# Performance work log

Measured on AMD Instinct MI355X. Metric: run time of the kernel, lower is better.

Reference implementation:

```python
import jax, jax.numpy as jnp
import numpy as np

T = 512           # num_timestamps
D = 512           # video_embed_dim
V = 2048          # fmri_dim (voxels)
H = 128           # hidden_dim


def setup_inputs() -> dict:
    key = jax.random.key(0)
    k = jax.random.split(key, 8)
    s1 = 1.0 / np.sqrt(D)
    s2 = 1.0 / np.sqrt(H)
    return {
        "video_embeddings": jax.random.normal(k[0], (T, D), dtype=jnp.float32),
        # stacked per-voxel weights (torch Linear: y = x @ W.T + b; we store W already transposed as [in, out])
        "W1": jax.random.uniform(k[1], (V, D, H), jnp.float32, -s1, s1),
        "b1": jax.random.uniform(k[2], (V, H), jnp.float32, -s1, s1),
        "W2": jax.random.uniform(k[3], (V, H, H), jnp.float32, -s2, s2),
        "b2": jax.random.uniform(k[4], (V, H), jnp.float32, -s2, s2),
        "W3": jax.random.uniform(k[5], (V, H), jnp.float32, -s2, s2),
        "b3": jax.random.uniform(k[6], (V,), jnp.float32, -s2, s2),
    }


def reference(video_embeddings, W1, b1, W2, b2, W3, b3):
    # Per-voxel MLP expressed as batched GEMMs over the voxel axis.
    # Dropout is identity in eval mode.
    h = jax.nn.relu(jnp.einsum("td,vdh->tvh", video_embeddings, W1) + b1)  # [T,V,H]
    h = jax.nn.relu(jnp.einsum("tvh,vhg->tvg", h, W2) + b2)                 # [T,V,H]
    out = jnp.einsum("tvh,vh->tv", h, W3) + b3                               # [T,V]
    return out
```

## Files before the change

kernel.cpp:

```cpp
#include <hip/hip_runtime.h>
#include <hip/hip_bf16.h>

#define TT 512
#define DD 512
#define VV 2048
#define HH 128

typedef __attribute__((ext_vector_type(8))) short bf16x8;
typedef __attribute__((ext_vector_type(8))) unsigned short ushort8;
typedef __attribute__((ext_vector_type(4))) unsigned short ushort4v;
typedef __attribute__((ext_vector_type(4))) float f32x4;

__device__ __forceinline__ unsigned short f2bf(float f) {
  union { __hip_bfloat16 b; unsigned short u; } cv;
  cv.b = __float2bfloat16(f);
  return cv.u;
}

__device__ __forceinline__ void lds_barrier() {
  asm volatile("s_waitcnt lgkmcnt(0)\n\ts_barrier" ::: "memory");
}

__global__ void cvt_x_kernel(const float* __restrict__ x, unsigned short* __restrict__ xb) {
  const int i = blockIdx.x * blockDim.x + threadIdx.x;
  const float4 f = ((const float4*)x)[i];
  ushort4v u;
  u[0] = f2bf(f.x); u[1] = f2bf(f.y); u[2] = f2bf(f.z); u[3] = f2bf(f.w);
  ((ushort4v*)xb)[i] = u;
}

__global__ __launch_bounds__(512, 2)
void voxel_mlp_kernel(const unsigned short* __restrict__ Xb,
                      const float* __restrict__ W1,
                      const float* __restrict__ b1,
                      const float* __restrict__ W2,
                      const float* __restrict__ b2,
                      const float* __restrict__ W3,
                      const float* __restrict__ b3,
                      float* __restrict__ out) {
  __shared__ __align__(16) char LDS[65536];
  constexpr unsigned W2BASE = 0;
  constexpr unsigned R1     = 32768;
  constexpr unsigned H1BASE = 32768;

  const int v   = blockIdx.x;
  const int tid = threadIdx.x;
  const int w   = tid >> 6;
  const int l   = tid & 63;
  const int lg  = l >> 4;
  const int ll  = l & 15;

  const float* W1v = W1 + (size_t)v * DD * HH;
  const float* W2v = W2 + (size_t)v * HH * HH;

  const int stago = (lg * 8) * HH + w * 16 + ll;
  const unsigned short* Xrow[4];
#pragma unroll
  for (int mi = 0; mi < 4; ++mi)
    Xrow[mi] = Xb + (size_t)(w * 64 + mi * 16 + ll) * DD + lg * 8;

  float w1s[4][8];
  float w2s[2][8];
  bf16x8 aS[2][4];

#define ISSUE_W1(t, slot)                                         \
  { const float* gp = W1v + stago + (t) * 32 * HH;                \
    _Pragma("unroll") for (int j = 0; j < 8; ++j)                 \
      w1s[slot][j] = gp[j * HH]; }

#define ISSUE_W2(t, slot)                                         \
  { const float* gp = W2v + stago + (t) * 32 * HH;                \
    _Pragma("unroll") for (int j = 0; j < 8; ++j)                 \
      w2s[slot][j] = gp[j * HH]; }

#define ISSUE_A(st, slot)                                         \
  { _Pragma("unroll") for (int mi = 0; mi < 4; ++mi)              \
      aS[slot][mi] = *(const bf16x8*)(Xrow[mi] + (st) * 32); }

#define CVT_W1(slot, dstByte)                                     \
  { ushort8 u;                                                    \
    _Pragma("unroll") for (int j = 0; j < 8; ++j)                 \
      u[j] = f2bf(w1s[slot][j]);                                  \
    *(ushort8*)(&LDS[(dstByte) + (unsigned)w * 1024u + (unsigned)l * 16u]) = u; }

#define CVT_W2(slot, dstByte)                                     \
  { ushort8 u;                                                    \
    _Pragma("unroll") for (int j = 0; j < 8; ++j)                 \
      u[j] = f2bf(w2s[slot][j]);                                  \
    *(ushort8*)(&LDS[(dstByte) + (unsigned)w * 1024u + (unsigned)l * 16u]) = u; }

  ISSUE_A(0, 0);
  ISSUE_W1(0, 0);
  ISSUE_W1(1, 1);
  ISSUE_W1(2, 2);
  CVT_W1(0, R1 + 0u * 8192u);
  lds_barrier();

  f32x4 acc1[4][8];
#pragma unroll
  for (int mi = 0; mi < 4; ++mi)
#pragma unroll
    for (int n = 0; n < 8; ++n) acc1[mi][n] = f32x4{0.f, 0.f, 0.f, 0.f};

#pragma unroll
  for (int s = 0; s < 16; ++s) {
    if (s + 1 < 16) ISSUE_A(s + 1, (s + 1) & 1);
    if (s + 3 < 16) ISSUE_W1(s + 3, (s + 3) & 3);

#pragma unroll
    for (int n = 0; n < 8; ++n) {
      const bf16x8 b = *(const bf16x8*)(&LDS[R1 + (unsigned)(s & 3) * 8192u + (unsigned)n * 1024u + (unsigned)l * 16u]);
#pragma unroll
      for (int mi = 0; mi < 4; ++mi)
        acc1[mi][n] = __builtin_amdgcn_mfma_f32_16x16x32_bf16(aS[s & 1][mi], b, acc1[mi][n], 0, 0, 0);
    }

    if (s < 15) CVT_W1((s + 1) & 3, R1 + (unsigned)((s + 1) & 3) * 8192u);

    if (s >= 2 && s < 6) CVT_W2(s & 1, W2BASE + (unsigned)(s - 2) * 8192u);
    if (s < 4) ISSUE_W2(s, s & 1);

    lds_barrier();
  }

#undef ISSUE_W1
#undef ISSUE_W2
#undef ISSUE_A
#undef CVT_W1
#undef CVT_W2

  float b1v[8], b2v[8], w3v[8];
#pragma unroll
  for (int n = 0; n < 8; ++n) {
    b1v[n] = b1[v * HH + n * 16 + ll];
    b2v[n] = b2[v * HH + n * 16 + ll];
    w3v[n] = W3[v * HH + n * 16 + ll];
  }
  const float b3v = b3[v];

  const unsigned slot = H1BASE + (unsigned)w * 4096u;

#pragma unroll
  for (int mi = 0; mi < 4; ++mi) {
#pragma unroll
    for (int n = 0; n < 8; ++n) {
#pragma unroll
      for (int r = 0; r < 4; ++r) {
        const int tl = lg * 4 + r;
        float hv = acc1[mi][n][r] + b1v[n];
        hv = fmaxf(hv, 0.f);
        const int h = n * 16 + ll;
        const unsigned byte = slot + (unsigned)tl * 256u + (unsigned)((h * 2) ^ ((tl & 7) << 4));
        *(unsigned short*)(&LDS[byte]) = f2bf(hv);
      }
    }
    f32x4 acc2[8];
#pragma unroll
    for (int n = 0; n < 8; ++n) acc2[n] = f32x4{0.f, 0.f, 0.f, 0.f};
#pragma unroll
    for (int ki = 0; ki < 4; ++ki) {
      const int k0 = ki * 32 + lg * 8;
      const unsigned abyte = slot + (unsigned)ll * 256u + (unsigned)((k0 * 2) ^ ((ll & 7) << 4));
      const bf16x8 a2 = *(const bf16x8*)(&LDS[abyte]);
#pragma unroll
      for (int n = 0; n < 8; ++n) {
        const bf16x8 bw = *(const bf16x8*)(&LDS[W2BASE + (unsigned)ki * 8192u + (unsigned)n * 1024u + (unsigned)l * 16u]);
        acc2[n] = __builtin_amdgcn_mfma_f32_16x16x32_bf16(a2, bw, acc2[n], 0, 0, 0);
      }
    }
#pragma unroll
    for (int r = 0; r < 4; ++r) {
      float p = 0.f;
#pragma unroll
      for (int n = 0; n < 8; ++n)
        p += fmaxf(acc2[n][r] + b2v[n], 0.f) * w3v[n];
      p += __shfl_xor(p, 1);
      p += __shfl_xor(p, 2);
      p += __shfl_xor(p, 4);
      p += __shfl_xor(p, 8);
      if (ll == 0) {
        const int t = w * 64 + mi * 16 + lg * 4 + r;
        out[t * VV + v] = p + b3v;
      }
    }
  }
}

extern "C" void kernel_launch(void* const* d_in, const int* in_sizes, int n_in,
                              void* d_out, int out_size, void* d_ws, size_t ws_size,
                              hipStream_t stream) {
  const float* X  = (const float*)d_in[0];
  const float* W1 = (const float*)d_in[1];
  const float* b1 = (const float*)d_in[2];
  const float* W2 = (const float*)d_in[3];
  const float* b2 = (const float*)d_in[4];
  const float* W3 = (const float*)d_in[5];
  const float* b3 = (const float*)d_in[6];
  float* out = (float*)d_out;

  unsigned short* Xb = (unsigned short*)d_ws;

  cvt_x_kernel<<<256, 256, 0, stream>>>(X, Xb);
  voxel_mlp_kernel<<<VV, 512, 0, stream>>>(Xb, W1, b1, W2, b2, W3, b3, out);
}
```

Measured before the change: 302.6 us.

## Split each voxel across four blocks by timestep quarter with XCD-aware mapping

Each voxel's work is now split over four blocks, each handling 128 of the 512 timesteps, so the grid grows from 2048 to 8192 blocks. Accumulator registers shrink by four, and launch bounds are raised to allow four blocks per CU. Block IDs are remapped so the four quarter-blocks of a voxel land on the same XCD, aiming for L2 reuse of that voxel's weights. The cost is that every block still loads and converts the full W1/W2 for its voxel, so weight reads and bf16 conversion are repeated four times, relying on L2 to absorb the extra traffic.

```diff
diff --git a/kernel.cpp b/kernel.cpp
--- a/kernel.cpp
+++ b/kernel.cpp
@@ -29,7 +29,7 @@
   ((ushort4v*)xb)[i] = u;
 }
 
-__global__ __launch_bounds__(512, 2)
+__global__ __launch_bounds__(512, 4)
 void voxel_mlp_kernel(const unsigned short* __restrict__ Xb,
                       const float* __restrict__ W1,
                       const float* __restrict__ b1,
@@ -43,7 +43,13 @@
   constexpr unsigned R1     = 32768;
   constexpr unsigned H1BASE = 32768;
 
-  const int v   = blockIdx.x;
+  const int bid = blockIdx.x;
+  const int xcd = bid & 7;
+  const int g   = bid >> 3;
+  const int v   = (g >> 2) * 8 + xcd;
+  const int q   = g & 3;
+  const int rowbase = q * 128;
+
   const int tid = threadIdx.x;
   const int w   = tid >> 6;
   const int l   = tid & 63;
@@ -54,14 +60,11 @@
   const float* W2v = W2 + (size_t)v * HH * HH;
 
   const int stago = (lg * 8) * HH + w * 16 + ll;
-  const unsigned short* Xrow[4];
-#pragma unroll
-  for (int mi = 0; mi < 4; ++mi)
-    Xrow[mi] = Xb + (size_t)(w * 64 + mi * 16 + ll) * DD + lg * 8;
+  const unsigned short* Xrow = Xb + (size_t)(rowbase + w * 16 + ll) * DD + lg * 8;
 
   float w1s[4][8];
   float w2s[2][8];
-  bf16x8 aS[2][4];
+  bf16x8 aS[2];
 
 #define ISSUE_W1(t, slot)                                         \
   { const float* gp = W1v + stago + (t) * 32 * HH;                \
@@ -74,8 +77,7 @@
       w2s[slot][j] = gp[j * HH]; }
 
 #define ISSUE_A(st, slot)                                         \
-  { _Pragma("unroll") for (int mi = 0; mi < 4; ++mi)              \
-      aS[slot][mi] = *(const bf16x8*)(Xrow[mi] + (st) * 32); }
+  { aS[slot] = *(const bf16x8*)(Xrow + (st) * 32); }
 
 #define CVT_W1(slot, dstByte)                                     \
   { ushort8 u;                                                    \
@@ -96,11 +98,9 @@
   CVT_W1(0, R1 + 0u * 8192u);
   lds_barrier();
 
-  f32x4 acc1[4][8];
-#pragma unroll
-  for (int mi = 0; mi < 4; ++mi)
-#pragma unroll
-    for (int n = 0; n < 8; ++n) acc1[mi][n] = f32x4{0.f, 0.f, 0.f, 0.f};
+  f32x4 acc1[8];
+#pragma unroll
+  for (int n = 0; n < 8; ++n) acc1[n] = f32x4{0.f, 0.f, 0.f, 0.f};
 
 #pragma unroll
   for (int s = 0; s < 16; ++s) {
@@ -110,9 +110,7 @@
 #pragma unroll
     for (int n = 0; n < 8; ++n) {
       const bf16x8 b = *(const bf16x8*)(&LDS[R1 + (unsigned)(s & 3) * 8192u + (unsigned)n * 1024u + (unsigned)l * 16u]);
-#pragma unroll
-      for (int mi = 0; mi < 4; ++mi)
-        acc1[mi][n] = __builtin_amdgcn_mfma_f32_16x16x32_bf16(aS[s & 1][mi], b, acc1[mi][n], 0, 0, 0);
+      acc1[n] = __builtin_amdgcn_mfma_f32_16x16x32_bf16(aS[s & 1], b, acc1[n], 0, 0, 0);
     }
 
     if (s < 15) CVT_W1((s + 1) & 3, R1 + (unsigned)((s + 1) & 3) * 8192u);
@@ -141,47 +139,44 @@
   const unsigned slot = H1BASE + (unsigned)w * 4096u;
 
 #pragma unroll
-  for (int mi = 0; mi < 4; ++mi) {
+  for (int n = 0; n < 8; ++n) {
+#pragma unroll
+    for (int r = 0; r < 4; ++r) {
+      const int tl = lg * 4 + r;
+      float hv = acc1[n][r] + b1v[n];
+      hv = fmaxf(hv, 0.f);
+      const int h = n * 16 + ll;
+      const unsigned byte = slot + (unsigned)tl * 256u + (unsigned)((h * 2) ^ ((tl & 7) << 4));
+      *(unsigned short*)(&LDS[byte]) = f2bf(hv);
+    }
+  }
+  f32x4 acc2[8];
+#pragma unroll
+  for (int n = 0; n < 8; ++n) acc2[n] = f32x4{0.f, 0.f, 0.f, 0.f};
+#pragma unroll
+  for (int ki = 0; ki < 4; ++ki) {
+    const int k0 = ki * 32 + lg * 8;
+    const unsigned abyte = slot + (unsigned)ll * 256u + (unsigned)((k0 * 2) ^ ((ll & 7) << 4));
+    const bf16x8 a2 = *(const bf16x8*)(&LDS[abyte]);
 #pragma unroll
     for (int n = 0; n < 8; ++n) {
-#pragma unroll
-      for (int r = 0; r < 4; ++r) {
-        const int tl = lg * 4 + r;
-        float hv = acc1[mi][n][r] + b1v[n];
-        hv = fmaxf(hv, 0.f);
-        const int h = n * 16 + ll;
-        const unsigned byte = slot + (unsigned)tl * 256u + (unsigned)((h * 2) ^ ((tl & 7) << 4));
-        *(unsigned short*)(&LDS[byte]) = f2bf(hv);
-      }
-    }
-    f32x4 acc2[8];
-#pragma unroll
-    for (int n = 0; n < 8; ++n) acc2[n] = f32x4{0.f, 0.f, 0.f, 0.f};
-#pragma unroll
-    for (int ki = 0; ki < 4; ++ki) {
-      const int k0 = ki * 32 + lg * 8;
-      const unsigned abyte = slot + (unsigned)ll * 256u + (unsigned)((k0 * 2) ^ ((ll & 7) << 4));
-      const bf16x8 a2 = *(const bf16x8*)(&LDS[abyte]);
-#pragma unroll
-      for (int n = 0; n < 8; ++n) {
-        const bf16x8 bw = *(const bf16x8*)(&LDS[W2BASE + (unsigned)ki * 8192u + (unsigned)n * 1024u + (unsigned)l * 16u]);
-        acc2[n] = __builtin_amdgcn_mfma_f32_16x16x32_bf16(a2, bw, acc2[n], 0, 0, 0);
-      }
-    }
-#pragma unroll
-    for (int r = 0; r < 4; ++r) {
-      float p = 0.f;
-#pragma unroll
-      for (int n = 0; n < 8; ++n)
-        p += fmaxf(acc2[n][r] + b2v[n], 0.f) * w3v[n];
-      p += __shfl_xor(p, 1);
-      p += __shfl_xor(p, 2);
-      p += __shfl_xor(p, 4);
-      p += __shfl_xor(p, 8);
-      if (ll == 0) {
-        const int t = w * 64 + mi * 16 + lg * 4 + r;
-        out[t * VV + v] = p + b3v;
-      }
+      const bf16x8 bw = *(const bf16x8*)(&LDS[W2BASE + (unsigned)ki * 8192u + (unsigned)n * 1024u + (unsigned)l * 16u]);
+      acc2[n] = __builtin_amdgcn_mfma_f32_16x16x32_bf16(a2, bw, acc2[n], 0, 0, 0);
+    }
+  }
+#pragma unroll
+  for (int r = 0; r < 4; ++r) {
+    float p = 0.f;
+#pragma unroll
+    for (int n = 0; n < 8; ++n)
+      p += fmaxf(acc2[n][r] + b2v[n], 0.f) * w3v[n];
+    p += __shfl_xor(p, 1);
+    p += __shfl_xor(p, 2);
+    p += __shfl_xor(p, 4);
+    p += __shfl_xor(p, 8);
+    if (ll == 0) {
+      const int t = rowbase + w * 16 + lg * 4 + r;
+      out[t * VV + v] = p + b3v;
     }
   }
 }
@@ -201,5 +196,5 @@
   unsigned short* Xb = (unsigned short*)d_ws;
 
   cvt_x_kernel<<<256, 256, 0, stream>>>(X, Xb);
-  voxel_mlp_kernel<<<VV, 512, 0, stream>>>(Xb, W1, b1, W2, b2, W3, b3, out);
-}
+  voxel_mlp_kernel<<<VV * 4, 512, 0, stream>>>(Xb, W1, b1, W2, b2, W3, b3, out);
+}
```

Result: slower. 353.9 us (+17.0%).

## Coalesce W1/W2 global loads with float2 rows and XOR-swizzled LDS staging

Applied to the files above, without the earlier changes.

Weight staging now has each lane read contiguous float2 pairs along the hidden dimension instead of one strided scalar per row, so global loads of W1 and W2 are coalesced. The bf16 tiles are written into LDS with an XOR swizzle, and the MFMA B-operand reads apply the matching swizzle to avoid bank conflicts. The K loop now covers 64 per stage with double-buffered 16KB LDS slots, and the X fragments are loaded directly at the start of each stage instead of being prefetched a stage ahead. This targets the HBM-bound weight streaming, at the cost of more complex indexing and less prefetch depth for X.

```diff
diff --git a/kernel.cpp b/kernel.cpp
--- a/kernel.cpp
+++ b/kernel.cpp
@@ -53,79 +53,87 @@
   const float* W1v = W1 + (size_t)v * DD * HH;
   const float* W2v = W2 + (size_t)v * HH * HH;
 
-  const int stago = (lg * 8) * HH + w * 16 + ll;
-  const unsigned short* Xrow[4];
+  const int      cn    = (l >> 3) & 7;
+  const unsigned xorv  = (unsigned)(cn & 7) << 4;
+  const unsigned wsl1  = (unsigned)(w >> 2) * 8192u + (unsigned)cn * 1024u;
+  const unsigned woff1 = ((unsigned)((w & 3) * 256 + (l & 7) * 32)) ^ xorv;
+  const unsigned wsl2  = (unsigned)cn * 1024u;
+  const unsigned woff2 = ((unsigned)((w >> 1) * 256 + (l & 7) * 32 + (w & 1) * 8)) ^ xorv;
+
+  float2 w1s[2][8];
+  float2 w2s[2][4];
+
+#define ISSUE_W1(t)                                                        \
+  { const float* gp = W1v + ((t) * 64 + w * 8) * HH + 2 * l;               \
+    _Pragma("unroll") for (int j = 0; j < 8; ++j)                          \
+      w1s[(t) & 1][j] = *(const float2*)(gp + j * HH); }
+
+#define CVT_W1(t)                                                          \
+  { ushort8 e0, e1;                                                        \
+    _Pragma("unroll") for (int j = 0; j < 8; ++j) {                        \
+      e0[j] = f2bf(w1s[(t) & 1][j].x);                                     \
+      e1[j] = f2bf(w1s[(t) & 1][j].y); }                                   \
+    const unsigned b_ = R1 + (unsigned)((t) & 1) * 16384u + wsl1;          \
+    *(ushort8*)(&LDS[b_ + woff1]) = e0;                                    \
+    *(ushort8*)(&LDS[b_ + (woff1 ^ 16u)]) = e1; }
+
+#define ISSUE_W2(s)                                                        \
+  { const float* gp = W2v + ((s) * 32 + w * 4) * HH + 2 * l;               \
+    _Pragma("unroll") for (int j = 0; j < 4; ++j)                          \
+      w2s[(s) & 1][j] = *(const float2*)(gp + j * HH); }
+
+#define CVT_W2(s)                                                          \
+  { ushort4v e0, e1;                                                       \
+    _Pragma("unroll") for (int j = 0; j < 4; ++j) {                        \
+      e0[j] = f2bf(w2s[(s) & 1][j].x);                                     \
+      e1[j] = f2bf(w2s[(s) & 1][j].y); }                                   \
+    const unsigned b_ = W2BASE + (unsigned)(s) * 8192u + wsl2;             \
+    *(ushort4v*)(&LDS[b_ + woff2]) = e0;                                   \
+    *(ushort4v*)(&LDS[b_ + (woff2 ^ 16u)]) = e1; }
+
+  ISSUE_W1(0);
+  ISSUE_W1(1);
+  CVT_W1(0);
+  lds_barrier();
+
+  f32x4 acc1[4][8];
 #pragma unroll
   for (int mi = 0; mi < 4; ++mi)
-    Xrow[mi] = Xb + (size_t)(w * 64 + mi * 16 + ll) * DD + lg * 8;
-
-  float w1s[4][8];
-  float w2s[2][8];
-  bf16x8 aS[2][4];
-
-#define ISSUE_W1(t, slot)                                         \
-  { const float* gp = W1v + stago + (t) * 32 * HH;                \
-    _Pragma("unroll") for (int j = 0; j < 8; ++j)                 \
-      w1s[slot][j] = gp[j * HH]; }
-
-#define ISSUE_W2(t, slot)                                         \
-  { const float* gp = W2v + stago + (t) * 32 * HH;                \
-    _Pragma("unroll") for (int j = 0; j < 8; ++j)                 \
-      w2s[slot][j] = gp[j * HH]; }
-
-#define ISSUE_A(st, slot)                                         \
-  { _Pragma("unroll") for (int mi = 0; mi < 4; ++mi)              \
-      aS[slot][mi] = *(const bf16x8*)(Xrow[mi] + (st) * 32); }
-
-#define CVT_W1(slot, dstByte)                                     \
-  { ushort8 u;                                                    \
-    _Pragma("unroll") for (int j = 0; j < 8; ++j)                 \
-      u[j] = f2bf(w1s[slot][j]);                                  \
-    *(ushort8*)(&LDS[(dstByte) + (unsigned)w * 1024u + (unsigned)l * 16u]) = u; }
-
-#define CVT_W2(slot, dstByte)                                     \
-  { ushort8 u;                                                    \
-    _Pragma("unroll") for (int j = 0; j < 8; ++j)                 \
-      u[j] = f2bf(w2s[slot][j]);                                  \
-    *(ushort8*)(&LDS[(dstByte) + (unsigned)w * 1024u + (unsigned)l * 16u]) = u; }
-
-  ISSUE_A(0, 0);
-  ISSUE_W1(0, 0);
-  ISSUE_W1(1, 1);
-  ISSUE_W1(2, 2);
-  CVT_W1(0, R1 + 0u * 8192u);
-  lds_barrier();
-
-  f32x4 acc1[4][8];
-#pragma unroll
-  for (int mi = 0; mi < 4; ++mi)
 #pragma unroll
     for (int n = 0; n < 8; ++n) acc1[mi][n] = f32x4{0.f, 0.f, 0.f, 0.f};
 
 #pragma unroll
-  for (int s = 0; s < 16; ++s) {
-    if (s + 1 < 16) ISSUE_A(s + 1, (s + 1) & 1);
-    if (s + 3 < 16) ISSUE_W1(s + 3, (s + 3) & 3);
-
-#pragma unroll
-    for (int n = 0; n < 8; ++n) {
-      const bf16x8 b = *(const bf16x8*)(&LDS[R1 + (unsigned)(s & 3) * 8192u + (unsigned)n * 1024u + (unsigned)l * 16u]);
+  for (int s = 0; s < 8; ++s) {
+    bf16x8 aS[2][4];
+#pragma unroll
+    for (int u = 0; u < 2; ++u)
 #pragma unroll
       for (int mi = 0; mi < 4; ++mi)
-        acc1[mi][n] = __builtin_amdgcn_mfma_f32_16x16x32_bf16(aS[s & 1][mi], b, acc1[mi][n], 0, 0, 0);
-    }
-
-    if (s < 15) CVT_W1((s + 1) & 3, R1 + (unsigned)((s + 1) & 3) * 8192u);
-
-    if (s >= 2 && s < 6) CVT_W2(s & 1, W2BASE + (unsigned)(s - 2) * 8192u);
-    if (s < 4) ISSUE_W2(s, s & 1);
-
+        aS[u][mi] = *(const bf16x8*)(Xb + (size_t)(w * 64 + mi * 16 + ll) * DD +
+                                     s * 64 + u * 32 + lg * 8);
+
+    if (s + 2 < 8) ISSUE_W1(s + 2);
+    if (s < 4)     ISSUE_W2(s);
+
+#pragma unroll
+    for (int u = 0; u < 2; ++u)
+#pragma unroll
+      for (int n = 0; n < 8; ++n) {
+        const bf16x8 b = *(const bf16x8*)(&LDS[R1 + (unsigned)(s & 1) * 16384u +
+                                               (unsigned)u * 8192u + (unsigned)n * 1024u +
+                                               (((unsigned)l * 16u) ^ ((unsigned)(n & 7) << 4))]);
+#pragma unroll
+        for (int mi = 0; mi < 4; ++mi)
+          acc1[mi][n] = __builtin_amdgcn_mfma_f32_16x16x32_bf16(aS[u][mi], b, acc1[mi][n], 0, 0, 0);
+      }
+
+    if (s < 7)            CVT_W1(s + 1);
+    if (s >= 1 && s <= 4) CVT_W2(s - 1);
     lds_barrier();
   }
 
 #undef ISSUE_W1
 #undef ISSUE_W2
-#undef ISSUE_A
 #undef CVT_W1
 #undef CVT_W2
 
@@ -150,30 +158,34 @@
         float hv = acc1[mi][n][r] + b1v[n];
         hv = fmaxf(hv, 0.f);
         const int h = n * 16 + ll;
-        const unsigned byte = slot + (unsigned)tl * 256u + (unsigned)((h * 2) ^ ((tl & 7) << 4));
+        const unsigned byte = slot + (unsigned)tl * 256u +
+                              (unsigned)((h * 2) ^ ((tl & 7) << 4));
         *(unsigned short*)(&LDS[byte]) = f2bf(hv);
       }
     }
     f32x4 acc2[8];
 #pragma unroll
-    for (int n = 0; n < 8; ++n) acc2[n] = f32x4{0.f, 0.f, 0.f, 0.f};
+    for (int m = 0; m < 8; ++m) acc2[m] = f32x4{0.f, 0.f, 0.f, 0.f};
 #pragma unroll
     for (int ki = 0; ki < 4; ++ki) {
       const int k0 = ki * 32 + lg * 8;
-      const unsigned abyte = slot + (unsigned)ll * 256u + (unsigned)((k0 * 2) ^ ((ll & 7) << 4));
+      const unsigned abyte = slot + (unsigned)ll * 256u +
+                             (unsigned)((k0 * 2) ^ ((ll & 7) << 4));
       const bf16x8 a2 = *(const bf16x8*)(&LDS[abyte]);
 #pragma unroll
-      for (int n = 0; n < 8; ++n) {
-        const bf16x8 bw = *(const bf16x8*)(&LDS[W2BASE + (unsigned)ki * 8192u + (unsigned)n * 1024u + (unsigned)l * 16u]);
-        acc2[n] = __builtin_amdgcn_mfma_f32_16x16x32_bf16(a2, bw, acc2[n], 0, 0, 0);
+      for (int m = 0; m < 8; ++m) {
+        const bf16x8 bw = *(const bf16x8*)(&LDS[W2BASE + (unsigned)ki * 8192u +
+                                                (unsigned)m * 1024u +
+                                                (((unsigned)l * 16u) ^ ((unsigned)(m & 7) << 4))]);
+        acc2[m] = __builtin_amdgcn_mfma_f32_16x16x32_bf16(a2, bw, acc2[m], 0, 0, 0);
       }
     }
 #pragma unroll
     for (int r = 0; r < 4; ++r) {
       float p = 0.f;
 #pragma unroll
-      for (int n = 0; n < 8; ++n)
-        p += fmaxf(acc2[n][r] + b2v[n], 0.f) * w3v[n];
+      for (int m = 0; m < 8; ++m)
+        p += fmaxf(acc2[m][r] + b2v[m], 0.f) * w3v[m];
       p += __shfl_xor(p, 1);
       p += __shfl_xor(p, 2);
       p += __shfl_xor(p, 4);
```

Result: no change. 305.6 us (+1.0%).
